# Kernel tuning notes

Hardware: AMD Instinct MI355X
Metric: run time of the kernel (lower is better)

## Reference

```python
import jax, jax.numpy as jnp
import numpy as np

RAD = 6371000.0   # earth radius [m]
OMEGA = 7.292e-5  # rotation rate [1/s]
CP = 1004.0


def _hgrad(f, coslat, dlat, dlon):
    # f: [B,Y,X] or [B,Y,X,Z]; centered diffs, periodic in lon, one-sided at lat edges
    cl = coslat.reshape((1, coslat.shape[0]) + (1,) * (f.ndim - 2))
    dfx = (jnp.roll(f, -1, axis=2) - jnp.roll(f, 1, axis=2)) / (2.0 * dlon * RAD * cl)
    dfy = (jnp.roll(f, -1, axis=1) - jnp.roll(f, 1, axis=1)) / (2.0 * dlat * RAD)
    dfy = dfy.at[:, 0].set((f[:, 1] - f[:, 0]) / (dlat * RAD))
    dfy = dfy.at[:, -1].set((f[:, -1] - f[:, -2]) / (dlat * RAD))
    return dfx, dfy


def _laplacian(f, coslat, dlat, dlon):
    cl = coslat.reshape((1, coslat.shape[0]) + (1,) * (f.ndim - 2))
    d2x = (jnp.roll(f, -1, axis=2) + jnp.roll(f, 1, axis=2) - 2.0 * f) / (dlon * RAD * cl) ** 2
    d2y = (jnp.roll(f, -1, axis=1) + jnp.roll(f, 1, axis=1) - 2.0 * f) / (dlat * RAD) ** 2
    d2y = d2y.at[:, 0].set(0.0).at[:, -1].set(0.0)
    return d2x + d2y


def _vgrad(f, ds):
    # d/dsigma on uniform sigma grid, centered interior, one-sided edges
    g = (jnp.roll(f, -1, axis=3) - jnp.roll(f, 1, axis=3)) / (2.0 * ds)
    g = g.at[..., 0].set((f[..., 1] - f[..., 0]) / ds)
    g = g.at[..., -1].set((f[..., -1] - f[..., -2]) / ds)
    return g


def _polar_filter(field, lat_rad):
    # zonal rFFT filter: cut wavenumbers k > K_max*cos(lat)
    f4 = field[..., None] if field.ndim == 3 else field
    B, Y, X, Z = f4.shape
    fc = jnp.fft.rfft(f4, axis=2)
    k = jnp.arange(fc.shape[2]).reshape(1, 1, -1, 1)
    cut = jnp.clip((X // 2) * jnp.cos(lat_rad), 1.0, None).reshape(1, Y, 1, 1)
    mask = (k <= cut).astype(f4.dtype)
    out = jnp.fft.irfft(fc * mask, n=X, axis=2)
    return out.reshape(field.shape)


def _dynamic_core(u, v, T, q, ps, g, R):
    B, Y, X, Z = u.shape
    dlat = jnp.pi / Y
    dlon = 2.0 * jnp.pi / X
    lat = (-jnp.pi / 2.0 + (jnp.arange(Y) + 0.5) * dlat).astype(u.dtype)
    coslat = jnp.cos(lat)
    fcor = (2.0 * OMEGA * jnp.sin(lat)).reshape(1, Y, 1, 1)

    # sigma coordinate: p = b_k * ps, uniform dsigma
    b_k = ((jnp.arange(Z) + 0.5) / Z).astype(u.dtype)         # [Z]
    ds = 1.0 / Z
    dsig = jnp.full((Z,), ds, dtype=u.dtype)
    p = b_k * ps[..., None]                                    # [B,Y,X,Z]
    # hydrostatic geopotential: integrate R*T dsigma/sigma from bottom (k=Z-1) up
    integ = R * T * (dsig / b_k)
    phi = jnp.cumsum(integ[..., ::-1], axis=-1)[..., ::-1]

    dudx, dudy = _hgrad(u, coslat, dlat, dlon)
    dvdx, dvdy = _hgrad(v, coslat, dlat, dlon)
    dTdx, dTdy = _hgrad(T, coslat, dlat, dlon)
    dphidx, dphidy = _hgrad(phi, coslat, dlat, dlon)
    dpsdx, dpsdy = _hgrad(ps, coslat, dlat, dlon)

    div_h = dudx + dvdy
    B_k = b_k.reshape(1, 1, 1, Z)
    DS = dsig.reshape(1, 1, 1, Z)

    mass_col = div_h * ps[..., None] + u * dpsdx[..., None] + v * dpsdy[..., None]
    dpsdt = -jnp.sum(mass_col * DS, axis=-1)                   # [B,Y,X]

    # sigma_dot: sig * int_0^1 M ds - int_0^sig M ds, over ps
    I = jnp.cumsum(mass_col * DS, axis=-1)
    sigma_dot = (B_k * I[..., -1:] - I) / (ps[..., None] + 1e-8)

    coriolis_u = fcor * v
    coriolis_v = -fcor * u
    pgf_u = -dphidx - R * T * B_k / (p + 1e-8) * dpsdx[..., None]
    pgf_v = -dphidy - R * T * B_k / (p + 1e-8) * dpsdy[..., None]

    h_adv_u = -(u * dudx + v * dudy)
    h_adv_v = -(u * dvdx + v * dvdy)
    v_adv_u = -sigma_dot * _vgrad(u, ds)
    v_adv_v = -sigma_dot * _vgrad(v, ds)
    h_adv_T = -(u * dTdx + v * dTdy)
    v_adv_T = -sigma_dot * _vgrad(T, ds)
    adiabatic_T = R * T / (p * CP + 1e-8) * (sigma_dot * ps[..., None])

    cos_factor = jnp.clip(coslat ** 2, 0.01, None).reshape(1, Y, 1, 1)
    nu_div = 500000.0 * cos_factor
    grad_div_u, grad_div_v = _hgrad(div_h, coslat, dlat, dlon)
    div_damp_u = nu_div * grad_div_u
    div_damp_v = nu_div * grad_div_v

    nu_h = 100000.0 * cos_factor
    diffusion_u = nu_h * _laplacian(u, coslat, dlat, dlon)
    diffusion_v = nu_h * _laplacian(v, coslat, dlat, dlon)
    diffusion_T = nu_h * _laplacian(T, coslat, dlat, dlon)

    r_fric = 1e-5
    dudt = h_adv_u + v_adv_u + coriolis_u + pgf_u + diffusion_u - r_fric * u + div_damp_u
    dvdt = h_adv_v + v_adv_v + coriolis_v + pgf_v + diffusion_v - r_fric * v + div_damp_v
    dTdt = h_adv_T + v_adv_T + adiabatic_T + diffusion_T

    dudt = jnp.clip(_polar_filter(dudt, lat), -0.02, 0.02)
    dvdt = jnp.clip(_polar_filter(dvdt, lat), -0.02, 0.02)
    dTdt = jnp.clip(_polar_filter(dTdt, lat), -0.01, 0.01)
    dpsdt = jnp.clip(_polar_filter(dpsdt, lat), -0.5, 0.5)
    dqdt = jnp.zeros_like(q)
    return dudt, dvdt, dTdt, dqdt, dpsdt


def setup_inputs() -> dict:
    key = jax.random.key(0)
    ks = jax.random.split(key, 5)
    B, Y, X, Z = 2, 360, 720, 32
    u = 10.0 * jax.random.normal(ks[0], (B, Y, X, Z), dtype=jnp.float32)
    v = 10.0 * jax.random.normal(ks[1], (B, Y, X, Z), dtype=jnp.float32)
    T = 220.0 + 80.0 * jax.random.uniform(ks[2], (B, Y, X, Z), dtype=jnp.float32)
    q = 0.02 * jax.random.uniform(ks[3], (B, Y, X, Z), dtype=jnp.float32)
    ps = 101325.0 * (0.95 + 0.1 * jax.random.uniform(ks[4], (B, Y, X), dtype=jnp.float32))
    return {"u": u, "v": v, "T": T, "q": q, "ps": ps,
            "g": jnp.float32(9.81), "R": jnp.float32(287.0)}


def reference(u, v, T, q, ps, g, R):
    return _dynamic_core(u, v, T, q, ps, g, R)
```

## Files before the change

### kernel.cpp

```cpp
#include <hip/hip_runtime.h>
#include <math.h>

#define NB 2
#define NY 360
#define NX 720
#define NZ 32
#define NPTS (NB*NY*NX*NZ)
#define NCOL (NB*NY*NX)

__device__ __forceinline__ int i4(int b,int y,int x,int z){ return (((b*NY)+y)*NX+x)*NZ+z; }
__device__ __forceinline__ int i3(int b,int y,int x){ return ((b*NY)+y)*NX+x; }

#define F_RAD   6371000.0f
#define F_OMEGA 7.292e-5f
#define F_CP    1004.0f
#define F_DLAT  ((float)(M_PI/360.0))
#define F_DYR   ((float)(M_PI/360.0*6371000.0))
#define F_HPI   ((float)(M_PI/2.0))
#define TH      ((float)(2.0*M_PI/720.0))

__global__ __launch_bounds__(256) void k_divh(const float* __restrict__ u,
                                              const float* __restrict__ v,
                                              float* __restrict__ divh) {
  const int bswz = (blockIdx.x & 7) * 2025 + (blockIdx.x >> 3);
  const int idx = bswz*256 + threadIdx.x;
  const int zq = idx & 7;
  const int x  = (idx >> 3) % NX;
  const int by = idx / (NX*8);
  const int y  = by % NY;
  const int b  = by / NY;
  const float lat = -F_HPI + (y+0.5f)*F_DLAT;
  const float cl  = cosf(lat);
  const float invdx = 0.5f/(F_DLAT*F_RAD*cl);
  const int xp = (x==NX-1)?0:x+1, xm = (x==0)?NX-1:x-1;
  const float4 uxp = *(const float4*)&u[i4(b,y,xp,zq*4)];
  const float4 uxm = *(const float4*)&u[i4(b,y,xm,zq*4)];
  float4 vyp, vym; float cy;
  if (y == 0)          { vyp = *(const float4*)&v[i4(b,1,x,zq*4)];    vym = *(const float4*)&v[i4(b,0,x,zq*4)];    cy = 1.0f/F_DYR; }
  else if (y == NY-1)  { vyp = *(const float4*)&v[i4(b,NY-1,x,zq*4)]; vym = *(const float4*)&v[i4(b,NY-2,x,zq*4)]; cy = 1.0f/F_DYR; }
  else                 { vyp = *(const float4*)&v[i4(b,y+1,x,zq*4)];  vym = *(const float4*)&v[i4(b,y-1,x,zq*4)];  cy = 0.5f/F_DYR; }
  float4 o;
  o.x = (uxp.x - uxm.x)*invdx + (vyp.x - vym.x)*cy;
  o.y = (uxp.y - uxm.y)*invdx + (vyp.y - vym.y)*cy;
  o.z = (uxp.z - uxm.z)*invdx + (vyp.z - vym.z)*cy;
  o.w = (uxp.w - uxm.w)*invdx + (vyp.w - vym.w)*cy;
  *(float4*)&divh[idx*4] = o;
}

__global__ __launch_bounds__(256) void k_tend(
    const float* __restrict__ u, const float* __restrict__ v,
    const float* __restrict__ T, const float* __restrict__ ps,
    const float* __restrict__ Rp, const float* __restrict__ divh,
    float* __restrict__ du, float* __restrict__ dv,
    float* __restrict__ dT, float* __restrict__ dps) {
  const int tid = threadIdx.x;
  const int z   = tid & 31;
  const int bswz = (blockIdx.x & 7) * 8100 + (blockIdx.x >> 3);
  const int col = bswz*8 + (tid>>5);
  const int x = col % NX;
  const int y = (col / NX) % NY;
  const int b = col / (NX*NY);
  const float R = Rp[0];

  const int xp = (x==NX-1)?0:x+1, xm = (x==0)?NX-1:x-1;
  const int ycm = (y>0)? y-1 : 0;
  const int ycp = (y<NY-1)? y+1 : NY-1;
  const bool y0 = (y==0), yN = (y==NY-1);

  const float lat  = -F_HPI + (y+0.5f)*F_DLAT;
  const float cl   = cosf(lat);
  const float fcor = 2.0f*F_OMEGA*sinf(lat);
  const float sx     = F_DLAT*F_RAD*cl;
  const float invdx  = 0.5f/sx;
  const float inv2dy = 0.5f/F_DYR;
  const float inv1dy = 1.0f/F_DYR;
  const float invsx2 = 1.0f/(sx*sx);
  const float invsy2 = 1.0f/(F_DYR*F_DYR);
  const float bk  = (z + 0.5f)/32.0f;
  const float dsv = 1.0f/32.0f;

  const int ic  = i4(b,y,x,z),   ixp = i4(b,y,xp,z), ixm = i4(b,y,xm,z);
  const int iyp = i4(b,ycp,x,z), iym = i4(b,ycm,x,z);

  const float uc=u[ic], uxp=u[ixp], uxm=u[ixm], uyp=u[iyp], uym=u[iym];
  const float vc=v[ic], vxp=v[ixp], vxm=v[ixm], vyp=v[iyp], vym=v[iym];
  const float Tc=T[ic], Txp=T[ixp], Txm=T[ixm], Typ=T[iyp], Tym=T[iym];
  const float Dc=divh[ic], Dxp=divh[ixp], Dxm=divh[ixm], Dyp=divh[iyp], Dym=divh[iym];
  const float psc=ps[i3(b,y,x)],   psxp=ps[i3(b,y,xp)], psxm=ps[i3(b,y,xm)];
  const float psyp=ps[i3(b,ycp,x)], psym=ps[i3(b,ycm,x)];

  auto dfy = [&](float fc_, float fyp_, float fym_) -> float {
    if (y0) return (fyp_ - fc_) * inv1dy;
    if (yN) return (fc_ - fym_) * inv1dy;
    return (fyp_ - fym_) * inv2dy;
  };
  auto lap = [&](float fc_, float fxp_, float fxm_, float fyp_, float fym_) -> float {
    float d2x = (fxp_ + fxm_ - 2.0f*fc_) * invsx2;
    float d2y = (y0||yN) ? 0.0f : (fyp_ + fym_ - 2.0f*fc_) * invsy2;
    return d2x + d2y;
  };
  auto sufscan = [&](float vv) -> float {
    #pragma unroll
    for (int d=1; d<32; d<<=1) { float t = __shfl_down(vv, d, 32); if (z+d<32) vv += t; }
    return vv;
  };
  auto prescan = [&](float vv) -> float {
    #pragma unroll
    for (int d=1; d<32; d<<=1) { float t = __shfl_up(vv, d, 32); if (z>=d) vv += t; }
    return vv;
  };
  auto vg = [&](float fc_) -> float {
    float fzp = __shfl_down(fc_,1,32), fzm = __shfl_up(fc_,1,32);
    if (z==0)  return (fzp - fc_) * 32.0f;
    if (z==31) return (fc_ - fzm) * 32.0f;
    return (fzp - fzm) * 16.0f;
  };

  const float dudx = (uxp-uxm)*invdx, dvdx = (vxp-vxm)*invdx, dTdx = (Txp-Txm)*invdx;
  const float dudy = dfy(uc,uyp,uym), dvdy_ = dfy(vc,vyp,vym), dTdy = dfy(Tc,Typ,Tym);
  const float dpsdx = (psxp-psxm)*invdx, dpsdy = dfy(psc,psyp,psym);
  const float gdivx = (Dxp-Dxm)*invdx,  gdivy = dfy(Dc,Dyp,Dym);

  const float rz = dsv / bk;
  const float dphidx = sufscan(R*rz*dTdx);
  const float dphidy = sufscan(R*rz*dTdy);

  const float mass = Dc*psc + uc*dpsdx + vc*dpsdy;
  float Ipre = prescan(mass) * dsv;
  const float Itot = __shfl(Ipre, 31, 32);
  const float sigd = (bk*Itot - Ipre) / (psc + 1e-8f);

  const float vgu = vg(uc), vgv = vg(vc), vgT = vg(Tc);

  const float pfac = R*Tc*bk/(bk*psc + 1e-8f);
  const float pgfu = -dphidx - pfac*dpsdx;
  const float pgfv = -dphidy - pfac*dpsdy;
  const float cf2  = fmaxf(cl*cl, 0.01f);
  const float nudiv = 500000.0f*cf2, nuh = 100000.0f*cf2;
  const float lapu = lap(uc,uxp,uxm,uyp,uym);
  const float lapv = lap(vc,vxp,vxm,vyp,vym);
  const float lapT = lap(Tc,Txp,Txm,Typ,Tym);
  const float adiab = R*Tc/(bk*psc*F_CP + 1e-8f) * (sigd*psc);

  float dut = -(uc*dudx + vc*dudy)  - sigd*vgu + fcor*vc + pgfu + nuh*lapu - 1e-5f*uc + nudiv*gdivx;
  float dvt = -(uc*dvdx + vc*dvdy_) - sigd*vgv - fcor*uc + pgfv + nuh*lapv - 1e-5f*vc + nudiv*gdivy;
  float dTt = -(uc*dTdx + vc*dTdy)  - sigd*vgT + adiab + nuh*lapT;

  du[ic] = dut; dv[ic] = dvt; dT[ic] = dTt;
  if (z == 0) dps[i3(b,y,x)] = -Itot;
}

__device__ __forceinline__ void filter_band(int y, int& k0, int& k1, bool& keepmode) {
  float lat = -F_HPI + (y+0.5f)*F_DLAT;
  float cut = fmaxf(360.0f*cosf(lat), 1.0f);
  int M = (int)floorf(cut);
  keepmode = (M <= 179);
  k0 = keepmode ? 0 : (M+1);
  k1 = keepmode ? M : 360;
}

#define FKMAX 180
__global__ __launch_bounds__(384, 4) void k_filter4b(
    float* __restrict__ du, float* __restrict__ dv, float* __restrict__ dT,
    float* __restrict__ dps, float* __restrict__ dq) {
  __shared__ __align__(16) float smem[8704];

  const int tid = threadIdx.x;
  const int xcd = blockIdx.x & 7;
  const int s   = blockIdx.x >> 3;
  const int bid = ((s >> 2) * 8 + xcd) * 4 + (s & 3);
  if (bid >= 9360) return;

  if (bid >= 8640) {
    float*  f  = smem;
    float2* tw = (float2*)(smem + 720);
    float*  sc = smem + 720 + 1440;
    float*  ss = sc + 184;
    const int row = bid - 8640;
    const int y = row % NY;
    float* base = dps + (size_t)row*NX;
    for (int t = tid; t < NX; t += 384) {
      float a = (float)t * TH;
      float sv, cv; sincosf(a, &sv, &cv);
      tw[t] = make_float2(cv, sv);
      f[t] = base[t];
    }
    int k0, k1; bool keepmode;
    filter_band(y, k0, k1, keepmode);
    const int nk = k1 - k0 + 1;
    __syncthreads();
    if (tid < nk) {
      const int k = k0 + tid;
      float ac=0.f, as=0.f; int idx=0;
      for (int xx=0; xx<NX; ++xx) {
        const float fv = f[xx];
        const float2 t2 = tw[idx];
        ac = fmaf(fv, t2.x, ac); as = fmaf(fv, t2.y, as);
        idx += k; if (idx >= NX) idx -= NX;
      }
      sc[tid]=ac; ss[tid]=as;
    }
    __syncthreads();
    if (tid < 360) {
      const int x0 = tid, x1 = tid + 360;
      const int t0 = (x0 * k0) % NX;
      const int t1 = (x1 * k0) % NX;
      float c0 = tw[t0].x, s0 = tw[t0].y;
      float c1 = tw[t1].x, s1 = tw[t1].y;
      const float dc0 = tw[x0].x, dn0 = tw[x0].y;
      const float dc1 = tw[x1].x, dn1 = tw[x1].y;
      float a0 = 0.f, a1 = 0.f;
      for (int kk = 0; kk < nk; ++kk) {
        const int k = k0 + kk;
        const float w = (k==0 || k==360) ? 1.0f : 2.0f;
        a0 = fmaf(sc[kk], w*c0, fmaf(ss[kk], w*s0, a0));
        a1 = fmaf(sc[kk], w*c1, fmaf(ss[kk], w*s1, a1));
        float n0 = c0*dc0 - s0*dn0; s0 = c0*dn0 + s0*dc0; c0 = n0;
        float n1 = c1*dc1 - s1*dn1; s1 = c1*dn1 + s1*dc1; c1 = n1;
      }
      const float inv = 1.0f/720.0f;
      float o0 = keepmode ? a0*inv : f[x0] - a0*inv;
      float o1 = keepmode ? a1*inv : f[x1] - a1*inv;
      o0 = fminf(fmaxf(o0, -0.5f), 0.5f);
      o1 = fminf(fmaxf(o1, -0.5f), 0.5f);
      base[x0] = o0;
      base[x1] = o1;
    }
    return;
  }

  float* S0p = smem + 0;
  float* S0m = smem + 728;
  float* S2p = smem + 1456;
  float* S2m = smem + 2184;
  float* Q1a = smem + 2912;
  float* Q2a = smem + 3640;
  float* Q3a = smem + 4368;
  float* Q4a = smem + 5096;
  float (*SD)[8][2] = (float(*)[8][2])(smem + 5824);

  {
    float4* dqv = (float4*)dq + (size_t)bid * 480;
    const float4 z4 = make_float4(0.f,0.f,0.f,0.f);
    for (int t = tid; t < 480; t += 384) dqv[t] = z4;
  }

  const int zq   = bid & 3;
  const int rest = bid >> 2;
  const int by   = rest % (NB*NY);
  const int fld  = rest / (NB*NY);
  const int y = by % NY, b = by / NY;
  float* fptr = (fld==0)? du : (fld==1)? dv : dT;
  const float clipv = (fld==2)? 0.01f : 0.02f;
  float* base = fptr + ((size_t)(b*NY+y)*NX)*NZ + zq*8;

  int k0, k1; bool keep;
  filter_band(y, k0, k1, keep);

  if (tid < 182) {
    const int p  = tid % 91;
    const int zh = tid / 91;
    const bool hasm = (p >= 1 && p <= 89);
    const int xm = 180 - p;
    const float4 q0 = *(const float4*)(base + (size_t)(p      )*NZ + zh*4);
    const float4 q1 = *(const float4*)(base + (size_t)(p + 180)*NZ + zh*4);
    const float4 q2 = *(const float4*)(base + (size_t)(p + 360)*NZ + zh*4);
    const float4 q3 = *(const float4*)(base + (size_t)(p + 540)*NZ + zh*4);
    float4 m0 = make_float4(0,0,0,0), m1 = m0, m2 = m0, m3 = m0;
    if (hasm) {
      m0 = *(const float4*)(base + (size_t)(xm      )*NZ + zh*4);
      m1 = *(const float4*)(base + (size_t)(xm + 180)*NZ + zh*4);
      m2 = *(const float4*)(base + (size_t)(xm + 360)*NZ + zh*4);
      m3 = *(const float4*)(base + (size_t)(xm + 540)*NZ + zh*4);
    }
    const int o = p*8 + zh*4;
    #pragma unroll
    for (int j = 0; j < 4; ++j) {
      const float a0 = (j==0)?q0.x:(j==1)?q0.y:(j==2)?q0.z:q0.w;
      const float a1 = (j==0)?q1.x:(j==1)?q1.y:(j==2)?q1.z:q1.w;
      const float a2 = (j==0)?q2.x:(j==1)?q2.y:(j==2)?q2.z:q2.w;
      const float a3 = (j==0)?q3.x:(j==1)?q3.y:(j==2)?q3.z:q3.w;
      const float b0 = (j==0)?m0.x:(j==1)?m0.y:(j==2)?m0.z:m0.w;
      const float b1 = (j==0)?m1.x:(j==1)?m1.y:(j==2)?m1.z:m1.w;
      const float b2 = (j==0)?m2.x:(j==1)?m2.y:(j==2)?m2.z:m2.w;
      const float b3 = (j==0)?m3.x:(j==1)?m3.y:(j==2)?m3.z:m3.w;
      const float s0  = a0+a1+a2+a3, s2  = a0-a1+a2-a3, A  = a0-a2, B  = a1-a3;
      const float s0M = b0+b1+b2+b3, s2M = b0-b1+b2-b3, AM = b0-b2, BM = b1-b3;
      S0p[o+j] = s0 + s0M;  S0m[o+j] = s0 - s0M;
      S2p[o+j] = s2 + s2M;  S2m[o+j] = s2 - s2M;
      Q1a[o+j] = A - BM;    Q2a[o+j] = AM - B;
      Q3a[o+j] = AM + B;    Q4a[o+j] = A + BM;
    }
  }
  __syncthreads();

  {
    const int xq = tid & 3;
    const int ks = tid >> 2;
    const bool isodd = (ks >= 48);
    const int slot = isodd ? ks - 48 : ks;
    const int ke0 = k0 + (k0 & 1);
    const int ko0 = k0 | 1;
    const int kbase = isodd ? ko0 : ke0;
    const int cnt   = (k1 >= kbase) ? (((k1 - kbase) >> 1) + 1) : 0;
    const bool dual = (cnt > 48);
    int k, x0, xe; bool act;
    if (dual) { k = kbase + 2*(slot + 48*(xq>>1)); x0 = (xq&1)?46:0; xe = (xq&1)?91:46; act = (k <= k1); }
    else      { k = kbase + 2*slot; x0 = 23*xq; xe = (xq==3)?91:(x0+23); act = (slot < cnt); }

    float ac[8], as[8];
    #pragma unroll
    for (int j=0;j<8;++j){ ac[j]=0.f; as[j]=0.f; }

    if (act) {
      float dc, ds; sincosf((float)k * TH, &ds, &dc);
      float c, s;   sincosf((float)((k * x0) % 720) * TH, &s, &c);
      const int n = xe - x0;
      if (!isodd) {
        const int r = k & 3;
        const float* Pc = ((r == 0) ? S0p : S2m) + x0*8;
        const float* Ps = ((r == 0) ? S0m : S2p) + x0*8;
        #pragma unroll 4
        for (int i = 0; i < n; ++i) {
          const float4 c0 = *(const float4*)(Pc + i*8);
          const float4 c1 = *(const float4*)(Pc + i*8 + 4);
          const float4 s0v = *(const float4*)(Ps + i*8);
          const float4 s1v = *(const float4*)(Ps + i*8 + 4);
          ac[0]=fmaf(c0.x ,c,ac[0]); as[0]=fmaf(s0v.x,s,as[0]);
          ac[1]=fmaf(c0.y ,c,ac[1]); as[1]=fmaf(s0v.y,s,as[1]);
          ac[2]=fmaf(c0.z ,c,ac[2]); as[2]=fmaf(s0v.z,s,as[2]);
          ac[3]=fmaf(c0.w ,c,ac[3]); as[3]=fmaf(s0v.w,s,as[3]);
          ac[4]=fmaf(c1.x ,c,ac[4]); as[4]=fmaf(s1v.x,s,as[4]);
          ac[5]=fmaf(c1.y ,c,ac[5]); as[5]=fmaf(s1v.y,s,as[5]);
          ac[6]=fmaf(c1.z ,c,ac[6]); as[6]=fmaf(s1v.z,s,as[6]);
          ac[7]=fmaf(c1.w ,c,ac[7]); as[7]=fmaf(s1v.w,s,as[7]);
          const float nc = fmaf(c, dc, -s*ds);
          s = fmaf(s, dc, c*ds); c = nc;
        }
      } else {
        const float sg = ((k & 3) == 1) ? 1.0f : -1.0f;
        const float* p1 = Q1a + x0*8; const float* p2 = Q2a + x0*8;
        const float* p3 = Q3a + x0*8; const float* p4 = Q4a + x0*8;
        #pragma unroll 2
        for (int i = 0; i < n; ++i) {
          const float4 u10 = *(const float4*)(p1 + i*8);
          const float4 u11 = *(const float4*)(p1 + i*8 + 4);
          const float4 u20 = *(const float4*)(p2 + i*8);
          const float4 u21 = *(const float4*)(p2 + i*8 + 4);
          const float4 u30 = *(const float4*)(p3 + i*8);
          const float4 u31 = *(const float4*)(p3 + i*8 + 4);
          const float4 u40 = *(const float4*)(p4 + i*8);
          const float4 u41 = *(const float4*)(p4 + i*8 + 4);
          const float svs = sg*s, cvs = sg*c;
          ac[0]=fmaf(u10.x,c,fmaf(u20.x,svs,ac[0])); as[0]=fmaf(u30.x,cvs,fmaf(u40.x,s,as[0]));
          ac[1]=fmaf(u10.y,c,fmaf(u20.y,svs,ac[1])); as[1]=fmaf(u30.y,cvs,fmaf(u40.y,s,as[1]));
          ac[2]=fmaf(u10.z,c,fmaf(u20.z,svs,ac[2])); as[2]=fmaf(u30.z,cvs,fmaf(u40.z,s,as[2]));
          ac[3]=fmaf(u10.w,c,fmaf(u20.w,svs,ac[3])); as[3]=fmaf(u30.w,cvs,fmaf(u40.w,s,as[3]));
          ac[4]=fmaf(u11.x,c,fmaf(u21.x,svs,ac[4])); as[4]=fmaf(u31.x,cvs,fmaf(u41.x,s,as[4]));
          ac[5]=fmaf(u11.y,c,fmaf(u21.y,svs,ac[5])); as[5]=fmaf(u31.y,cvs,fmaf(u41.y,s,as[5]));
          ac[6]=fmaf(u11.z,c,fmaf(u21.z,svs,ac[6])); as[6]=fmaf(u31.z,cvs,fmaf(u41.z,s,as[6]));
          ac[7]=fmaf(u11.w,c,fmaf(u21.w,svs,ac[7])); as[7]=fmaf(u31.w,cvs,fmaf(u41.w,s,as[7]));
          const float nc = fmaf(c, dc, -s*ds);
          s = fmaf(s, dc, c*ds); c = nc;
        }
      }
    }
    #pragma unroll
    for (int j=0;j<8;++j){
      ac[j] += __shfl_xor(ac[j], 1);
      as[j] += __shfl_xor(as[j], 1);
    }
    if (!dual) {
      #pragma unroll
      for (int j=0;j<8;++j){
        ac[j] += __shfl_xor(ac[j], 2);
        as[j] += __shfl_xor(as[j], 2);
      }
    }
    if (act && ((xq & (dual ? 1 : 3)) == 0)) {
      const float w = (k==0 || k==360) ? 1.0f : 2.0f;
      const int r = k - k0;
      *(float4*)&SD[r][0][0] = make_float4(w*ac[0], w*as[0], w*ac[1], w*as[1]);
      *(float4*)&SD[r][2][0] = make_float4(w*ac[2], w*as[2], w*ac[3], w*as[3]);
      *(float4*)&SD[r][4][0] = make_float4(w*ac[4], w*as[4], w*ac[5], w*as[5]);
      *(float4*)&SD[r][6][0] = make_float4(w*ac[6], w*as[6], w*ac[7], w*as[7]);
    }
  }
  __syncthreads();

  if (tid < 182) {
    const int p  = tid % 91;
    const int zh = tid / 91;
    const bool hasm = (p >= 1 && p <= 89);
    float lx0[4],lx1[4],lx2[4],lx3[4], lm0[4],lm1[4],lm2[4],lm3[4];
    #pragma unroll
    for (int j=0;j<4;++j){ lx0[j]=lx1[j]=lx2[j]=lx3[j]=0.f; lm0[j]=lm1[j]=lm2[j]=lm3[j]=0.f; }

    const int m4 = (4*p) % 720;
    float dstep_s, dstep_c; sincosf((float)m4 * TH, &dstep_s, &dstep_c);

    #pragma unroll
    for (int ri = 0; ri < 2; ++ri) {
      const int r = ri*2;
      const float tau = (ri==0)? 1.0f : -1.0f;
      const int kst = k0 + ((r - (k0 & 3) + 4) & 3);
      if (kst > k1) continue;
      float P[4]={0,0,0,0}, S[4]={0,0,0,0};
      float sv, cv; sincosf((float)((kst * p) % 720) * TH, &sv, &cv);
      #pragma unroll 2
      for (int k = kst; k <= k1; k += 4) {
        const float4 d01 = *(const float4*)&SD[k - k0][zh*4 + 0][0];
        const float4 d23 = *(const float4*)&SD[k - k0][zh*4 + 2][0];
        P[0]=fmaf(d01.x,cv,P[0]); S[0]=fmaf(d01.y,sv,S[0]);
        P[1]=fmaf(d01.z,cv,P[1]); S[1]=fmaf(d01.w,sv,S[1]);
        P[2]=fmaf(d23.x,cv,P[2]); S[2]=fmaf(d23.y,sv,S[2]);
        P[3]=fmaf(d23.z,cv,P[3]); S[3]=fmaf(d23.w,sv,S[3]);
        float nc = fmaf(cv, dstep_c, -sv*dstep_s);
        float ns = fmaf(sv, dstep_c,  cv*dstep_s);
        cv = nc; sv = ns;
      }
      #pragma unroll
      for (int j=0;j<4;++j){
        const float hx = P[j] + S[j];
        const float hm = (ri==0) ? (P[j] - S[j]) : (S[j] - P[j]);
        lx0[j]+=hx; lx2[j]+=hx; lx1[j]+=tau*hx; lx3[j]+=tau*hx;
        lm0[j]+=hm; lm2[j]+=hm; lm1[j]+=tau*hm; lm3[j]+=tau*hm;
      }
    }
    #pragma unroll
    for (int ri = 0; ri < 2; ++ri) {
      const int r = ri*2 + 1;
      const float sig = (ri==0)? 1.0f : -1.0f;
      const int kst = k0 + ((r - (k0 & 3) + 4) & 3);
      if (kst > k1) continue;
      float Cc[4]={0,0,0,0}, Cs[4]={0,0,0,0}, Sc[4]={0,0,0,0}, Ss[4]={0,0,0,0};
      float sv, cv; sincosf((float)((kst * p) % 720) * TH, &sv, &cv);
      #pragma unroll 2
      for (int k = kst; k <= k1; k += 4) {
        const float4 d01 = *(const float4*)&SD[k - k0][zh*4 + 0][0];
        const float4 d23 = *(const float4*)&SD[k - k0][zh*4 + 2][0];
        Cc[0]=fmaf(d01.x,cv,Cc[0]); Cs[0]=fmaf(d01.x,sv,Cs[0]);
        Sc[0]=fmaf(d01.y,cv,Sc[0]); Ss[0]=fmaf(d01.y,sv,Ss[0]);
        Cc[1]=fmaf(d01.z,cv,Cc[1]); Cs[1]=fmaf(d01.z,sv,Cs[1]);
        Sc[1]=fmaf(d01.w,cv,Sc[1]); Ss[1]=fmaf(d01.w,sv,Ss[1]);
        Cc[2]=fmaf(d23.x,cv,Cc[2]); Cs[2]=fmaf(d23.x,sv,Cs[2]);
        Sc[2]=fmaf(d23.y,cv,Sc[2]); Ss[2]=fmaf(d23.y,sv,Ss[2]);
        Cc[3]=fmaf(d23.z,cv,Cc[3]); Cs[3]=fmaf(d23.z,sv,Cs[3]);
        Sc[3]=fmaf(d23.w,cv,Sc[3]); Ss[3]=fmaf(d23.w,sv,Ss[3]);
        float nc = fmaf(cv, dstep_c, -sv*dstep_s);
        float ns = fmaf(sv, dstep_c,  cv*dstep_s);
        cv = nc; sv = ns;
      }
      #pragma unroll
      for (int j=0;j<4;++j){
        const float hrx = Cc[j] + Ss[j];
        const float hix = Sc[j] - Cs[j];
        const float hrm = sig*(Cs[j] + Sc[j]);
        const float him = Ss[j] - Cc[j];
        lx0[j]+=hrx; lx2[j]-=hrx; lx1[j]+=sig*hix; lx3[j]-=sig*hix;
        lm0[j]+=hrm; lm2[j]-=hrm; lm1[j]+=him;     lm3[j]-=him;
      }
    }

    const float inv = 1.0f/720.0f;
    float qx[4][4], qm[4][4];
    if (!keep) {
      const int o = p*8 + zh*4;
      #pragma unroll
      for (int j=0;j<4;++j){
        const float s0x = 0.5f*(S0p[o+j] + S0m[o+j]);
        const float s0M = 0.5f*(S0p[o+j] - S0m[o+j]);
        const float s2x = 0.5f*(S2p[o+j] + S2m[o+j]);
        const float s2M = 0.5f*(S2p[o+j] - S2m[o+j]);
        const float Ax  = 0.5f*(Q1a[o+j] + Q4a[o+j]);
        const float AM  = 0.5f*(Q2a[o+j] + Q3a[o+j]);
        const float Bx  = 0.5f*(Q3a[o+j] - Q2a[o+j]);
        const float BM  = 0.5f*(Q4a[o+j] - Q1a[o+j]);
        { const float sp = 0.25f*(s0x + s2x), sm = 0.25f*(s0x - s2x);
          qx[0][j] = sp + 0.5f*Ax; qx[1][j] = sm + 0.5f*Bx;
          qx[2][j] = sp - 0.5f*Ax; qx[3][j] = sm - 0.5f*Bx; }
        { const float sp = 0.25f*(s0M + s2M), sm = 0.25f*(s0M - s2M);
          qm[0][j] = sp + 0.5f*AM; qm[1][j] = sm + 0.5f*BM;
          qm[2][j] = sp - 0.5f*AM; qm[3][j] = sm - 0.5f*BM; }
      }
    }
    {
      float o[4][4];
      #pragma unroll
      for (int j=0;j<4;++j){
        float l0 = lx0[j]*inv, l1 = lx1[j]*inv, l2 = lx2[j]*inv, l3 = lx3[j]*inv;
        if (!keep) { l0 = qx[0][j]-l0; l1 = qx[1][j]-l1; l2 = qx[2][j]-l2; l3 = qx[3][j]-l3; }
        o[0][j] = fminf(fmaxf(l0,-clipv),clipv);
        o[1][j] = fminf(fmaxf(l1,-clipv),clipv);
        o[2][j] = fminf(fmaxf(l2,-clipv),clipv);
        o[3][j] = fminf(fmaxf(l3,-clipv),clipv);
      }
      #pragma unroll
      for (int jj=0;jj<4;++jj)
        *(float4*)(base + (size_t)(p + 180*jj)*NZ + zh*4) =
            make_float4(o[jj][0], o[jj][1], o[jj][2], o[jj][3]);
    }
    if (hasm) {
      const int xm = 180 - p;
      float o[4][4];
      #pragma unroll
      for (int j=0;j<4;++j){
        float l0 = lm0[j]*inv, l1 = lm1[j]*inv, l2 = lm2[j]*inv, l3 = lm3[j]*inv;
        if (!keep) { l0 = qm[0][j]-l0; l1 = qm[1][j]-l1; l2 = qm[2][j]-l2; l3 = qm[3][j]-l3; }
        o[0][j] = fminf(fmaxf(l0,-clipv),clipv);
        o[1][j] = fminf(fmaxf(l1,-clipv),clipv);
        o[2][j] = fminf(fmaxf(l2,-clipv),clipv);
        o[3][j] = fminf(fmaxf(l3,-clipv),clipv);
      }
      #pragma unroll
      for (int jj=0;jj<4;++jj)
        *(float4*)(base + (size_t)(xm + 180*jj)*NZ + zh*4) =
            make_float4(o[jj][0], o[jj][1], o[jj][2], o[jj][3]);
    }
  }
}

extern "C" void kernel_launch(void* const* d_in, const int* in_sizes, int n_in,
                              void* d_out, int out_size, void* d_ws, size_t ws_size,
                              hipStream_t stream) {
  (void)in_sizes; (void)n_in; (void)d_ws; (void)ws_size; (void)out_size;
  const float* u  = (const float*)d_in[0];
  const float* v  = (const float*)d_in[1];
  const float* T  = (const float*)d_in[2];
  const float* ps = (const float*)d_in[4];
  const float* Rp = (const float*)d_in[6];

  float* out = (float*)d_out;
  float* du  = out;
  float* dv  = out + (size_t)NPTS;
  float* dT  = out + (size_t)2*NPTS;
  float* dq  = out + (size_t)3*NPTS;
  float* dps = out + (size_t)4*NPTS;

  k_divh<<<NPTS/(256*4), 256, 0, stream>>>(u, v, dq);
  k_tend<<<NCOL/8,       256, 0, stream>>>(u, v, T, ps, Rp, dq, du, dv, dT, dps);
  k_filter4b<<<9376, 384, 0, stream>>>(du, dv, dT, dps, dq);
}
```

Baseline: 434.4 us.

## Vectorize tendency kernel to four levels per thread; spread filter DFT over more threads

The tendency kernel now gives each thread four vertical levels, using float4 loads and stores and an 8-lane shuffle scan with in-register partial sums in place of a 32-lane shuffle scan. Column and per-column setup work (trig, ps loads) is amortized over more levels, and there are fewer instructions per byte. Separately, the filter kernel's inverse-DFT phase now uses 364 of 384 threads, each handling 2 levels instead of 4, which raises parallelism but halves per-thread reuse of the twiddle recurrence. Register pressure in the tendency kernel rises.

Result: slower. 477.3 us (+9.9%).

```diff
diff --git a/kernel.cpp b/kernel.cpp
--- a/kernel.cpp
+++ b/kernel.cpp
@@ -54,9 +54,9 @@
     float* __restrict__ du, float* __restrict__ dv,
     float* __restrict__ dT, float* __restrict__ dps) {
   const int tid = threadIdx.x;
-  const int z   = tid & 31;
-  const int bswz = (blockIdx.x & 7) * 8100 + (blockIdx.x >> 3);
-  const int col = bswz*8 + (tid>>5);
+  const int zl  = tid & 7;
+  const int bswz = (blockIdx.x & 7) * 2025 + (blockIdx.x >> 3);
+  const int col = bswz*32 + (tid>>3);
   const int x = col % NX;
   const int y = (col / NX) % NY;
   const int b = col / (NX*NY);
@@ -76,78 +76,146 @@
   const float inv1dy = 1.0f/F_DYR;
   const float invsx2 = 1.0f/(sx*sx);
   const float invsy2 = 1.0f/(F_DYR*F_DYR);
-  const float bk  = (z + 0.5f)/32.0f;
   const float dsv = 1.0f/32.0f;
-
-  const int ic  = i4(b,y,x,z),   ixp = i4(b,y,xp,z), ixm = i4(b,y,xm,z);
-  const int iyp = i4(b,ycp,x,z), iym = i4(b,ycm,x,z);
-
-  const float uc=u[ic], uxp=u[ixp], uxm=u[ixm], uyp=u[iyp], uym=u[iym];
-  const float vc=v[ic], vxp=v[ixp], vxm=v[ixm], vyp=v[iyp], vym=v[iym];
-  const float Tc=T[ic], Txp=T[ixp], Txm=T[ixm], Typ=T[iyp], Tym=T[iym];
-  const float Dc=divh[ic], Dxp=divh[ixp], Dxm=divh[ixm], Dyp=divh[iyp], Dym=divh[iym];
+  const int zb = zl*4;
+  float bk[4];
+  #pragma unroll
+  for (int j=0;j<4;++j) bk[j] = (zb + j + 0.5f)/32.0f;
+
+  const int ic  = i4(b,y,x,zb),   ixp = i4(b,y,xp,zb), ixm = i4(b,y,xm,zb);
+  const int iyp = i4(b,ycp,x,zb), iym = i4(b,ycm,x,zb);
+
   const float psc=ps[i3(b,y,x)],   psxp=ps[i3(b,y,xp)], psxm=ps[i3(b,y,xm)];
   const float psyp=ps[i3(b,ycp,x)], psym=ps[i3(b,ycm,x)];
 
-  auto dfy = [&](float fc_, float fyp_, float fym_) -> float {
+  auto dfy1 = [&](float fc_, float fyp_, float fym_) -> float {
     if (y0) return (fyp_ - fc_) * inv1dy;
     if (yN) return (fc_ - fym_) * inv1dy;
     return (fyp_ - fym_) * inv2dy;
   };
-  auto lap = [&](float fc_, float fxp_, float fxm_, float fyp_, float fym_) -> float {
+  auto lap1 = [&](float fc_, float fxp_, float fxm_, float fyp_, float fym_) -> float {
     float d2x = (fxp_ + fxm_ - 2.0f*fc_) * invsx2;
     float d2y = (y0||yN) ? 0.0f : (fyp_ + fym_ - 2.0f*fc_) * invsy2;
     return d2x + d2y;
   };
-  auto sufscan = [&](float vv) -> float {
-    #pragma unroll
-    for (int d=1; d<32; d<<=1) { float t = __shfl_down(vv, d, 32); if (z+d<32) vv += t; }
-    return vv;
+  auto suf32 = [&](const float vv[4], float out[4]) {
+    const float s3 = vv[3], s2 = vv[2]+s3, s1 = vv[1]+s2, s0 = vv[0]+s1;
+    float S = s0;
+    { float t=__shfl_down(S,1,8); if (zl+1<8) S+=t; }
+    { float t=__shfl_down(S,2,8); if (zl+2<8) S+=t; }
+    { float t=__shfl_down(S,4,8); if (zl+4<8) S+=t; }
+    const float hi = S - s0;
+    out[0]=s0+hi; out[1]=s1+hi; out[2]=s2+hi; out[3]=s3+hi;
   };
-  auto prescan = [&](float vv) -> float {
-    #pragma unroll
-    for (int d=1; d<32; d<<=1) { float t = __shfl_up(vv, d, 32); if (z>=d) vv += t; }
-    return vv;
+  auto pre32 = [&](const float vv[4], float out[4], float& tot) {
+    const float p0 = vv[0], p1 = vv[1]+p0, p2 = vv[2]+p1, p3 = vv[3]+p2;
+    float P = p3;
+    { float t=__shfl_up(P,1,8); if (zl>=1) P+=t; }
+    { float t=__shfl_up(P,2,8); if (zl>=2) P+=t; }
+    { float t=__shfl_up(P,4,8); if (zl>=4) P+=t; }
+    const float lo = P - p3;
+    out[0]=p0+lo; out[1]=p1+lo; out[2]=p2+lo; out[3]=p3+lo;
+    tot = __shfl(P, 7, 8);
   };
-  auto vg = [&](float fc_) -> float {
-    float fzp = __shfl_down(fc_,1,32), fzm = __shfl_up(fc_,1,32);
-    if (z==0)  return (fzp - fc_) * 32.0f;
-    if (z==31) return (fc_ - fzm) * 32.0f;
-    return (fzp - fzm) * 16.0f;
+  auto vg4 = [&](const float c[4], float out[4]) {
+    const float up = __shfl_up(c[3], 1, 8);
+    const float dn = __shfl_down(c[0], 1, 8);
+    out[0] = (zl==0) ? (c[1]-c[0])*32.0f : (c[1]-up)*16.0f;
+    out[1] = (c[2]-c[0])*16.0f;
+    out[2] = (c[3]-c[1])*16.0f;
+    out[3] = (zl==7) ? (c[3]-c[2])*32.0f : (dn-c[2])*16.0f;
   };
-
-  const float dudx = (uxp-uxm)*invdx, dvdx = (vxp-vxm)*invdx, dTdx = (Txp-Txm)*invdx;
-  const float dudy = dfy(uc,uyp,uym), dvdy_ = dfy(vc,vyp,vym), dTdy = dfy(Tc,Typ,Tym);
-  const float dpsdx = (psxp-psxm)*invdx, dpsdy = dfy(psc,psyp,psym);
-  const float gdivx = (Dxp-Dxm)*invdx,  gdivy = dfy(Dc,Dyp,Dym);
-
-  const float rz = dsv / bk;
-  const float dphidx = sufscan(R*rz*dTdx);
-  const float dphidy = sufscan(R*rz*dTdy);
-
-  const float mass = Dc*psc + uc*dpsdx + vc*dpsdy;
-  float Ipre = prescan(mass) * dsv;
-  const float Itot = __shfl(Ipre, 31, 32);
-  const float sigd = (bk*Itot - Ipre) / (psc + 1e-8f);
-
-  const float vgu = vg(uc), vgv = vg(vc), vgT = vg(Tc);
-
-  const float pfac = R*Tc*bk/(bk*psc + 1e-8f);
-  const float pgfu = -dphidx - pfac*dpsdx;
-  const float pgfv = -dphidy - pfac*dpsdy;
+  auto unpack = [](const float4 f, float a[4]) { a[0]=f.x; a[1]=f.y; a[2]=f.z; a[3]=f.w; };
+
+  float ucv[4], dudx[4], dudy[4], lapu[4], vgu[4];
+  {
+    float c[4],a[4],m[4],p[4],q[4];
+    unpack(*(const float4*)&u[ic],c);  unpack(*(const float4*)&u[ixp],a);
+    unpack(*(const float4*)&u[ixm],m); unpack(*(const float4*)&u[iyp],p);
+    unpack(*(const float4*)&u[iym],q);
+    #pragma unroll
+    for (int j=0;j<4;++j){ ucv[j]=c[j]; dudx[j]=(a[j]-m[j])*invdx;
+      dudy[j]=dfy1(c[j],p[j],q[j]); lapu[j]=lap1(c[j],a[j],m[j],p[j],q[j]); }
+    vg4(ucv, vgu);
+  }
+  float vcv[4], dvdx[4], dvdy[4], lapv[4], vgv[4];
+  {
+    float c[4],a[4],m[4],p[4],q[4];
+    unpack(*(const float4*)&v[ic],c);  unpack(*(const float4*)&v[ixp],a);
+    unpack(*(const float4*)&v[ixm],m); unpack(*(const float4*)&v[iyp],p);
+    unpack(*(const float4*)&v[iym],q);
+    #pragma unroll
+    for (int j=0;j<4;++j){ vcv[j]=c[j]; dvdx[j]=(a[j]-m[j])*invdx;
+      dvdy[j]=dfy1(c[j],p[j],q[j]); lapv[j]=lap1(c[j],a[j],m[j],p[j],q[j]); }
+    vg4(vcv, vgv);
+  }
+  float Tcv[4], dTdx[4], dTdy[4], lapT[4], vgT[4];
+  {
+    float c[4],a[4],m[4],p[4],q[4];
+    unpack(*(const float4*)&T[ic],c);  unpack(*(const float4*)&T[ixp],a);
+    unpack(*(const float4*)&T[ixm],m); unpack(*(const float4*)&T[iyp],p);
+    unpack(*(const float4*)&T[iym],q);
+    #pragma unroll
+    for (int j=0;j<4;++j){ Tcv[j]=c[j]; dTdx[j]=(a[j]-m[j])*invdx;
+      dTdy[j]=dfy1(c[j],p[j],q[j]); lapT[j]=lap1(c[j],a[j],m[j],p[j],q[j]); }
+    vg4(Tcv, vgT);
+  }
+  float Dcv[4], gdivx[4], gdivy[4];
+  {
+    float c[4],a[4],m[4],p[4],q[4];
+    unpack(*(const float4*)&divh[ic],c);  unpack(*(const float4*)&divh[ixp],a);
+    unpack(*(const float4*)&divh[ixm],m); unpack(*(const float4*)&divh[iyp],p);
+    unpack(*(const float4*)&divh[iym],q);
+    #pragma unroll
+    for (int j=0;j<4;++j){ Dcv[j]=c[j]; gdivx[j]=(a[j]-m[j])*invdx;
+      gdivy[j]=dfy1(c[j],p[j],q[j]); }
+  }
+
+  const float dpsdx = (psxp-psxm)*invdx;
+  const float dpsdy = dfy1(psc,psyp,psym);
+
+  float dphidx[4], dphidy[4];
+  {
+    float a[4], bvv[4];
+    #pragma unroll
+    for (int j=0;j<4;++j){ const float rz = R*dsv/bk[j]; a[j]=rz*dTdx[j]; bvv[j]=rz*dTdy[j]; }
+    suf32(a, dphidx);
+    suf32(bvv, dphidy);
+  }
+
+  float mass[4], Ipre[4], tot;
+  #pragma unroll
+  for (int j=0;j<4;++j) mass[j] = Dcv[j]*psc + ucv[j]*dpsdx + vcv[j]*dpsdy;
+  pre32(mass, Ipre, tot);
+  const float Itot = tot * dsv;
+  float sigd[4];
+  #pragma unroll
+  for (int j=0;j<4;++j) sigd[j] = (bk[j]*Itot - Ipre[j]*dsv) / (psc + 1e-8f);
+
   const float cf2  = fmaxf(cl*cl, 0.01f);
   const float nudiv = 500000.0f*cf2, nuh = 100000.0f*cf2;
-  const float lapu = lap(uc,uxp,uxm,uyp,uym);
-  const float lapv = lap(vc,vxp,vxm,vyp,vym);
-  const float lapT = lap(Tc,Txp,Txm,Typ,Tym);
-  const float adiab = R*Tc/(bk*psc*F_CP + 1e-8f) * (sigd*psc);
-
-  float dut = -(uc*dudx + vc*dudy)  - sigd*vgu + fcor*vc + pgfu + nuh*lapu - 1e-5f*uc + nudiv*gdivx;
-  float dvt = -(uc*dvdx + vc*dvdy_) - sigd*vgv - fcor*uc + pgfv + nuh*lapv - 1e-5f*vc + nudiv*gdivy;
-  float dTt = -(uc*dTdx + vc*dTdy)  - sigd*vgT + adiab + nuh*lapT;
-
-  du[ic] = dut; dv[ic] = dvt; dT[ic] = dTt;
-  if (z == 0) dps[i3(b,y,x)] = -Itot;
+
+  float4 odu, odv, odT;
+  float outu[4], outv[4], outT[4];
+  #pragma unroll
+  for (int j=0;j<4;++j){
+    const float pfac = R*Tcv[j]*bk[j]/(bk[j]*psc + 1e-8f);
+    const float pgfu = -dphidx[j] - pfac*dpsdx;
+    const float pgfv = -dphidy[j] - pfac*dpsdy;
+    const float adiab = R*Tcv[j]/(bk[j]*psc*F_CP + 1e-8f) * (sigd[j]*psc);
+    outu[j] = -(ucv[j]*dudx[j] + vcv[j]*dudy[j]) - sigd[j]*vgu[j] + fcor*vcv[j] + pgfu
+              + nuh*lapu[j] - 1e-5f*ucv[j] + nudiv*gdivx[j];
+    outv[j] = -(ucv[j]*dvdx[j] + vcv[j]*dvdy[j]) - sigd[j]*vgv[j] - fcor*ucv[j] + pgfv
+              + nuh*lapv[j] - 1e-5f*vcv[j] + nudiv*gdivy[j];
+    outT[j] = -(ucv[j]*dTdx[j] + vcv[j]*dTdy[j]) - sigd[j]*vgT[j] + adiab + nuh*lapT[j];
+  }
+  odu = make_float4(outu[0],outu[1],outu[2],outu[3]);
+  odv = make_float4(outv[0],outv[1],outv[2],outv[3]);
+  odT = make_float4(outT[0],outT[1],outT[2],outT[3]);
+  *(float4*)&du[ic] = odu;
+  *(float4*)&dv[ic] = odv;
+  *(float4*)&dT[ic] = odT;
+  if (zl == 0) dps[col] = -Itot;
 }
 
 __device__ __forceinline__ void filter_band(int y, int& k0, int& k1, bool& keepmode) {
@@ -257,33 +325,33 @@
   int k0, k1; bool keep;
   filter_band(y, k0, k1, keep);
 
-  if (tid < 182) {
+  if (tid < 364) {
     const int p  = tid % 91;
-    const int zh = tid / 91;
+    const int zp = tid / 91;
     const bool hasm = (p >= 1 && p <= 89);
     const int xm = 180 - p;
-    const float4 q0 = *(const float4*)(base + (size_t)(p      )*NZ + zh*4);
-    const float4 q1 = *(const float4*)(base + (size_t)(p + 180)*NZ + zh*4);
-    const float4 q2 = *(const float4*)(base + (size_t)(p + 360)*NZ + zh*4);
-    const float4 q3 = *(const float4*)(base + (size_t)(p + 540)*NZ + zh*4);
-    float4 m0 = make_float4(0,0,0,0), m1 = m0, m2 = m0, m3 = m0;
+    const float2 q0 = *(const float2*)(base + (size_t)(p      )*NZ + zp*2);
+    const float2 q1 = *(const float2*)(base + (size_t)(p + 180)*NZ + zp*2);
+    const float2 q2 = *(const float2*)(base + (size_t)(p + 360)*NZ + zp*2);
+    const float2 q3 = *(const float2*)(base + (size_t)(p + 540)*NZ + zp*2);
+    float2 m0 = make_float2(0,0), m1 = m0, m2 = m0, m3 = m0;
     if (hasm) {
-      m0 = *(const float4*)(base + (size_t)(xm      )*NZ + zh*4);
-      m1 = *(const float4*)(base + (size_t)(xm + 180)*NZ + zh*4);
-      m2 = *(const float4*)(base + (size_t)(xm + 360)*NZ + zh*4);
-      m3 = *(const float4*)(base + (size_t)(xm + 540)*NZ + zh*4);
-    }
-    const int o = p*8 + zh*4;
-    #pragma unroll
-    for (int j = 0; j < 4; ++j) {
-      const float a0 = (j==0)?q0.x:(j==1)?q0.y:(j==2)?q0.z:q0.w;
-      const float a1 = (j==0)?q1.x:(j==1)?q1.y:(j==2)?q1.z:q1.w;
-      const float a2 = (j==0)?q2.x:(j==1)?q2.y:(j==2)?q2.z:q2.w;
-      const float a3 = (j==0)?q3.x:(j==1)?q3.y:(j==2)?q3.z:q3.w;
-      const float b0 = (j==0)?m0.x:(j==1)?m0.y:(j==2)?m0.z:m0.w;
-      const float b1 = (j==0)?m1.x:(j==1)?m1.y:(j==2)?m1.z:m1.w;
-      const float b2 = (j==0)?m2.x:(j==1)?m2.y:(j==2)?m2.z:m2.w;
-      const float b3 = (j==0)?m3.x:(j==1)?m3.y:(j==2)?m3.z:m3.w;
+      m0 = *(const float2*)(base + (size_t)(xm      )*NZ + zp*2);
+      m1 = *(const float2*)(base + (size_t)(xm + 180)*NZ + zp*2);
+      m2 = *(const float2*)(base + (size_t)(xm + 360)*NZ + zp*2);
+      m3 = *(const float2*)(base + (size_t)(xm + 540)*NZ + zp*2);
+    }
+    const int o = p*8 + zp*2;
+    #pragma unroll
+    for (int j = 0; j < 2; ++j) {
+      const float a0 = (j==0)?q0.x:q0.y;
+      const float a1 = (j==0)?q1.x:q1.y;
+      const float a2 = (j==0)?q2.x:q2.y;
+      const float a3 = (j==0)?q3.x:q3.y;
+      const float b0 = (j==0)?m0.x:m0.y;
+      const float b1 = (j==0)?m1.x:m1.y;
+      const float b2 = (j==0)?m2.x:m2.y;
+      const float b3 = (j==0)?m3.x:m3.y;
       const float s0  = a0+a1+a2+a3, s2  = a0-a1+a2-a3, A  = a0-a2, B  = a1-a3;
       const float s0M = b0+b1+b2+b3, s2M = b0-b1+b2-b3, AM = b0-b2, BM = b1-b3;
       S0p[o+j] = s0 + s0M;  S0m[o+j] = s0 - s0M;
@@ -388,13 +456,13 @@
   }
   __syncthreads();
 
-  if (tid < 182) {
+  if (tid < 364) {
     const int p  = tid % 91;
-    const int zh = tid / 91;
+    const int zp = tid / 91;
     const bool hasm = (p >= 1 && p <= 89);
-    float lx0[4],lx1[4],lx2[4],lx3[4], lm0[4],lm1[4],lm2[4],lm3[4];
-    #pragma unroll
-    for (int j=0;j<4;++j){ lx0[j]=lx1[j]=lx2[j]=lx3[j]=0.f; lm0[j]=lm1[j]=lm2[j]=lm3[j]=0.f; }
+    float lx0[2],lx1[2],lx2[2],lx3[2], lm0[2],lm1[2],lm2[2],lm3[2];
+    #pragma unroll
+    for (int j=0;j<2;++j){ lx0[j]=lx1[j]=lx2[j]=lx3[j]=0.f; lm0[j]=lm1[j]=lm2[j]=lm3[j]=0.f; }
 
     const int m4 = (4*p) % 720;
     float dstep_s, dstep_c; sincosf((float)m4 * TH, &dstep_s, &dstep_c);
@@ -405,22 +473,19 @@
       const float tau = (ri==0)? 1.0f : -1.0f;
       const int kst = k0 + ((r - (k0 & 3) + 4) & 3);
       if (kst > k1) continue;
-      float P[4]={0,0,0,0}, S[4]={0,0,0,0};
+      float P[2]={0,0}, S[2]={0,0};
       float sv, cv; sincosf((float)((kst * p) % 720) * TH, &sv, &cv);
       #pragma unroll 2
       for (int k = kst; k <= k1; k += 4) {
-        const float4 d01 = *(const float4*)&SD[k - k0][zh*4 + 0][0];
-        const float4 d23 = *(const float4*)&SD[k - k0][zh*4 + 2][0];
-        P[0]=fmaf(d01.x,cv,P[0]); S[0]=fmaf(d01.y,sv,S[0]);
-        P[1]=fmaf(d01.z,cv,P[1]); S[1]=fmaf(d01.w,sv,S[1]);
-        P[2]=fmaf(d23.x,cv,P[2]); S[2]=fmaf(d23.y,sv,S[2]);
-        P[3]=fmaf(d23.z,cv,P[3]); S[3]=fmaf(d23.w,sv,S[3]);
+        const float4 d = *(const float4*)&SD[k - k0][zp*2][0];
+        P[0]=fmaf(d.x,cv,P[0]); S[0]=fmaf(d.y,sv,S[0]);
+        P[1]=fmaf(d.z,cv,P[1]); S[1]=fmaf(d.w,sv,S[1]);
         float nc = fmaf(cv, dstep_c, -sv*dstep_s);
         float ns = fmaf(sv, dstep_c,  cv*dstep_s);
         cv = nc; sv = ns;
       }
       #pragma unroll
-      for (int j=0;j<4;++j){
+      for (int j=0;j<2;++j){
         const float hx = P[j] + S[j];
         const float hm = (ri==0) ? (P[j] - S[j]) : (S[j] - P[j]);
         lx0[j]+=hx; lx2[j]+=hx; lx1[j]+=tau*hx; lx3[j]+=tau*hx;
@@ -433,26 +498,21 @@
       const float sig = (ri==0)? 1.0f : -1.0f;
       const int kst = k0 + ((r - (k0 & 3) + 4) & 3);
       if (kst > k1) continue;
-      float Cc[4]={0,0,0,0}, Cs[4]={0,0,0,0}, Sc[4]={0,0,0,0}, Ss[4]={0,0,0,0};
+      float Cc[2]={0,0}, Cs[2]={0,0}, Sc[2]={0,0}, Ss[2]={0,0};
       float sv, cv; sincosf((float)((kst * p) % 720) * TH, &sv, &cv);
       #pragma unroll 2
       for (int k = kst; k <= k1; k += 4) {
-        const float4 d01 = *(const float4*)&SD[k - k0][zh*4 + 0][0];
-        const float4 d23 = *(const float4*)&SD[k - k0][zh*4 + 2][0];
-        Cc[0]=fmaf(d01.x,cv,Cc[0]); Cs[0]=fmaf(d01.x,sv,Cs[0]);
-        Sc[0]=fmaf(d01.y,cv,Sc[0]); Ss[0]=fmaf(d01.y,sv,Ss[0]);
-        Cc[1]=fmaf(d01.z,cv,Cc[1]); Cs[1]=fmaf(d01.z,sv,Cs[1]);
-        Sc[1]=fmaf(d01.w,cv,Sc[1]); Ss[1]=fmaf(d01.w,sv,Ss[1]);
-        Cc[2]=fmaf(d23.x,cv,Cc[2]); Cs[2]=fmaf(d23.x,sv,Cs[2]);
-        Sc[2]=fmaf(d23.y,cv,Sc[2]); Ss[2]=fmaf(d23.y,sv,Ss[2]);
-        Cc[3]=fmaf(d23.z,cv,Cc[3]); Cs[3]=fmaf(d23.z,sv,Cs[3]);
-        Sc[3]=fmaf(d23.w,cv,Sc[3]); Ss[3]=fmaf(d23.w,sv,Ss[3]);
+        const float4 d = *(const float4*)&SD[k - k0][zp*2][0];
+        Cc[0]=fmaf(d.x,cv,Cc[0]); Cs[0]=fmaf(d.x,sv,Cs[0]);
+        Sc[0]=fmaf(d.y,cv,Sc[0]); Ss[0]=fmaf(d.y,sv,Ss[0]);
+        Cc[1]=fmaf(d.z,cv,Cc[1]); Cs[1]=fmaf(d.z,sv,Cs[1]);
+        Sc[1]=fmaf(d.w,cv,Sc[1]); Ss[1]=fmaf(d.w,sv,Ss[1]);
         float nc = fmaf(cv, dstep_c, -sv*dstep_s);
         float ns = fmaf(sv, dstep_c,  cv*dstep_s);
         cv = nc; sv = ns;
       }
       #pragma unroll
-      for (int j=0;j<4;++j){
+      for (int j=0;j<2;++j){
         const float hrx = Cc[j] + Ss[j];
         const float hix = Sc[j] - Cs[j];
         const float hrm = sig*(Cs[j] + Sc[j]);
@@ -463,11 +523,11 @@
     }
 
     const float inv = 1.0f/720.0f;
-    float qx[4][4], qm[4][4];
+    float qx[4][2], qm[4][2];
     if (!keep) {
-      const int o = p*8 + zh*4;
-      #pragma unroll
-      for (int j=0;j<4;++j){
+      const int o = p*8 + zp*2;
+      #pragma unroll
+      for (int j=0;j<2;++j){
         const float s0x = 0.5f*(S0p[o+j] + S0m[o+j]);
         const float s0M = 0.5f*(S0p[o+j] - S0m[o+j]);
         const float s2x = 0.5f*(S2p[o+j] + S2m[o+j]);
@@ -485,9 +545,9 @@
       }
     }
     {
-      float o[4][4];
-      #pragma unroll
-      for (int j=0;j<4;++j){
+      float o[4][2];
+      #pragma unroll
+      for (int j=0;j<2;++j){
         float l0 = lx0[j]*inv, l1 = lx1[j]*inv, l2 = lx2[j]*inv, l3 = lx3[j]*inv;
         if (!keep) { l0 = qx[0][j]-l0; l1 = qx[1][j]-l1; l2 = qx[2][j]-l2; l3 = qx[3][j]-l3; }
         o[0][j] = fminf(fmaxf(l0,-clipv),clipv);
@@ -497,14 +557,13 @@
       }
       #pragma unroll
       for (int jj=0;jj<4;++jj)
-        *(float4*)(base + (size_t)(p + 180*jj)*NZ + zh*4) =
-            make_float4(o[jj][0], o[jj][1], o[jj][2], o[jj][3]);
+        *(float2*)(base + (size_t)(p + 180*jj)*NZ + zp*2) = make_float2(o[jj][0], o[jj][1]);
     }
     if (hasm) {
       const int xm = 180 - p;
-      float o[4][4];
-      #pragma unroll
-      for (int j=0;j<4;++j){
+      float o[4][2];
+      #pragma unroll
+      for (int j=0;j<2;++j){
         float l0 = lm0[j]*inv, l1 = lm1[j]*inv, l2 = lm2[j]*inv, l3 = lm3[j]*inv;
         if (!keep) { l0 = qm[0][j]-l0; l1 = qm[1][j]-l1; l2 = qm[2][j]-l2; l3 = qm[3][j]-l3; }
         o[0][j] = fminf(fmaxf(l0,-clipv),clipv);
@@ -514,8 +573,7 @@
       }
       #pragma unroll
       for (int jj=0;jj<4;++jj)
-        *(float4*)(base + (size_t)(xm + 180*jj)*NZ + zh*4) =
-            make_float4(o[jj][0], o[jj][1], o[jj][2], o[jj][3]);
+        *(float2*)(base + (size_t)(xm + 180*jj)*NZ + zp*2) = make_float2(o[jj][0], o[jj][1]);
     }
   }
 }
@@ -538,6 +596,6 @@
   float* dps = out + (size_t)4*NPTS;
 
   k_divh<<<NPTS/(256*4), 256, 0, stream>>>(u, v, dq);
-  k_tend<<<NCOL/8,       256, 0, stream>>>(u, v, T, ps, Rp, dq, du, dv, dT, dps);
+  k_tend<<<NCOL/32,      256, 0, stream>>>(u, v, T, ps, Rp, dq, du, dv, dT, dps);
   k_filter4b<<<9376, 384, 0, stream>>>(du, dv, dT, dps, dq);
 }
```
